# Kernel tuning notes

Measured on AMD Instinct MI355X. Metric: run time of the kernel, lower is better.

Reference implementation:

```python
import jax, jax.numpy as jnp
import numpy as np
import math

EPS = 1e-06
C_CONST = 2.0 + EPS
CHUNK = 128


def _features(xc, omega, W_poly, quad_nodes):
    # xc: (B,H,t,D) -> poly:(B,H,t,P), prf:(R,B,H,t,M)
    xn = xc / jnp.clip(jnp.linalg.norm(xc, axis=-1, keepdims=True), 1e-12)  # F.normalize
    poly = jnp.einsum('bhtd,hdp->bhtp', xn, W_poly)
    proj = jnp.einsum('bhtd,rhdm->rbhtm', xn, omega)
    s = quad_nodes[:, None, None, None, None]
    sqrt2s = jnp.sqrt(2.0 * jnp.clip(s, 0.0))
    M = omega.shape[-1]
    prf = jnp.exp(jnp.clip(proj * sqrt2s - s, -20.0, 20.0)) / math.sqrt(M)
    return poly, prf


def setup_inputs() -> dict:
    key = jax.random.key(0)
    ks = jax.random.split(key, 6)
    B, T, E, H, D, M, R, P = 1, 1024, 512, 8, 64, 8, 1, 32
    x = jax.random.normal(ks[0], (B, T, E), jnp.float32)
    W_qkv = jax.random.normal(ks[1], (3 * E, E), jnp.float32) / math.sqrt(E)
    b_qkv = jnp.zeros((3 * E,), jnp.float32)
    W_out = jax.random.normal(ks[2], (E, E), jnp.float32) / math.sqrt(E)
    b_out = jnp.zeros((E,), jnp.float32)
    omega = jax.random.normal(ks[3], (R, H, D, M), jnp.float32)
    W_poly = jax.random.normal(ks[4], (H, D, P), jnp.float32) / math.sqrt(D)
    nodes, weights = np.polynomial.laguerre.laggauss(R)
    quad_nodes = jnp.asarray(nodes, jnp.float32) / C_CONST
    quad_weights = jnp.asarray(weights, jnp.float32) / C_CONST
    return {"x": x, "W_qkv": W_qkv, "b_qkv": b_qkv, "W_out": W_out, "b_out": b_out,
            "omega": omega, "W_poly": W_poly, "quad_nodes": quad_nodes, "quad_weights": quad_weights}


def reference(x, W_qkv, b_qkv, W_out, b_out, omega, W_poly, quad_nodes, quad_weights):
    B, T, E = x.shape
    R, H, D, M = omega.shape
    P = W_poly.shape[-1]
    qkv = x @ W_qkv.T + b_qkv
    q, k, v = jnp.split(qkv, 3, axis=-1)

    def to_chunks(a):
        # (B,T,E) -> (Nc,B,H,chunk,D)
        return a.reshape(B, T, H, D).transpose(0, 2, 1, 3).reshape(B, H, T // CHUNK, CHUNK, D).transpose(2, 0, 1, 3, 4)

    qc, kc, vc = map(to_chunks, (q, k, v))
    sqw = jnp.sqrt(jnp.clip(quad_weights, 0.0))[:, None, None, None, None]
    kv0 = jnp.zeros((R, B, H, P, M, D), jnp.float32)
    k0 = jnp.zeros((R, B, H, P, M), jnp.float32)

    def step(carry, inp):
        kv_state, k_state = carry
        qch, kch, vch = inp
        q_poly, q_prf = _features(qch, omega, W_poly, quad_nodes)
        k_poly, k_prf = _features(kch, omega, W_poly, quad_nodes)
        q_prf = q_prf * sqw
        k_prf = k_prf * sqw
        q_outer = jnp.einsum('bhtp,rbhtm->rbhtpm', q_poly, q_prf)
        k_outer = jnp.einsum('bhtp,rbhtm->rbhtpm', k_poly, k_prf)
        kv_prod = jnp.einsum('rbhtpm,bhtd->rbhtpmd', k_outer, vch)
        kv_cur = jnp.cumsum(kv_prod, axis=3) + kv_state[:, :, :, None]
        k_cur = jnp.cumsum(k_outer, axis=3) + k_state[:, :, :, None]
        ctx = jnp.einsum('rbhtpm,rbhtpmd->bhtd', q_outer, kv_cur)  # sums over r too
        den = jnp.einsum('rbhtpm,rbhtpm->bht', q_outer, k_cur)
        out = ctx / jnp.clip(den, 1e-06)[..., None]
        return (kv_cur[:, :, :, -1], k_cur[:, :, :, -1]), out

    _, outs = jax.lax.scan(step, (kv0, k0), (qc, kc, vc))  # (Nc,B,H,chunk,D)
    out = outs.transpose(1, 2, 0, 3, 4).reshape(B, H, T, D).transpose(0, 2, 1, 3).reshape(B, T, E)
    return out @ W_out.T + b_out
```

## Files before the change

kernel.cpp:

```cpp
#include <hip/hip_runtime.h>
#include <math.h>


__global__ __launch_bounds__(256) void gemm_part_kernel(
    const float* __restrict__ A, const float* __restrict__ W,
    float* __restrict__ part, int M, int N, int K, int Kc)
{
    __shared__ float a_t[2][16][68];
    __shared__ float w_t[2][16][68];
    const int tid = threadIdx.x;
    const int n0 = blockIdx.x * 64;
    const int m0 = blockIdx.y * 64;
    const int sk = blockIdx.z;
    const int kb = sk * Kc;
    const int tx = tid & 15, ty = tid >> 4;
    const int lrow = tid >> 2;
    const int lk4  = (tid & 3) * 4;
    float acc[4][4];
#pragma unroll
    for (int i = 0; i < 4; ++i)
#pragma unroll
        for (int j = 0; j < 4; ++j) acc[i][j] = 0.f;

    const float* Ap = &A[(m0 + lrow) * K + kb + lk4];
    const float* Wp = &W[(n0 + lrow) * K + kb + lk4];
    float4 ra = *(const float4*)Ap;
    float4 rw = *(const float4*)Wp;
    a_t[0][lk4 + 0][lrow] = ra.x; a_t[0][lk4 + 1][lrow] = ra.y;
    a_t[0][lk4 + 2][lrow] = ra.z; a_t[0][lk4 + 3][lrow] = ra.w;
    w_t[0][lk4 + 0][lrow] = rw.x; w_t[0][lk4 + 1][lrow] = rw.y;
    w_t[0][lk4 + 2][lrow] = rw.z; w_t[0][lk4 + 3][lrow] = rw.w;
    __syncthreads();

    int cur = 0;
    for (int k0 = 16; k0 <= Kc; k0 += 16) {
        const bool more = (k0 < Kc);
        if (more) {
            ra = *(const float4*)(Ap + k0);
            rw = *(const float4*)(Wp + k0);
        }
#pragma unroll
        for (int k = 0; k < 16; ++k) {
            float4 af = *(const float4*)&a_t[cur][k][ty * 4];
            float4 wf = *(const float4*)&w_t[cur][k][tx * 4];
            acc[0][0] += af.x * wf.x; acc[0][1] += af.x * wf.y;
            acc[0][2] += af.x * wf.z; acc[0][3] += af.x * wf.w;
            acc[1][0] += af.y * wf.x; acc[1][1] += af.y * wf.y;
            acc[1][2] += af.y * wf.z; acc[1][3] += af.y * wf.w;
            acc[2][0] += af.z * wf.x; acc[2][1] += af.z * wf.y;
            acc[2][2] += af.z * wf.z; acc[2][3] += af.z * wf.w;
            acc[3][0] += af.w * wf.x; acc[3][1] += af.w * wf.y;
            acc[3][2] += af.w * wf.z; acc[3][3] += af.w * wf.w;
        }
        if (more) {
            const int nxt = cur ^ 1;
            a_t[nxt][lk4 + 0][lrow] = ra.x; a_t[nxt][lk4 + 1][lrow] = ra.y;
            a_t[nxt][lk4 + 2][lrow] = ra.z; a_t[nxt][lk4 + 3][lrow] = ra.w;
            w_t[nxt][lk4 + 0][lrow] = rw.x; w_t[nxt][lk4 + 1][lrow] = rw.y;
            w_t[nxt][lk4 + 2][lrow] = rw.z; w_t[nxt][lk4 + 3][lrow] = rw.w;
            __syncthreads();
            cur = nxt;
        }
    }
#pragma unroll
    for (int i = 0; i < 4; ++i) {
        float4 o = make_float4(acc[i][0], acc[i][1], acc[i][2], acc[i][3]);
        *(float4*)&part[((size_t)sk * M + m0 + ty * 4 + i) * N + n0 + tx * 4] = o;
    }
}

__global__ __launch_bounds__(256) void reduce_bias_kernel(
    const float* __restrict__ part, const float* __restrict__ bias,
    float* __restrict__ C, int MN, int N, int S)
{
    const int i4 = (blockIdx.x * 256 + threadIdx.x) * 4;
    if (i4 >= MN) return;
    float4 acc = *(const float4*)&part[i4];
    for (int s = 1; s < S; ++s) {
        float4 p = *(const float4*)&part[(size_t)s * MN + i4];
        acc.x += p.x; acc.y += p.y; acc.z += p.z; acc.w += p.w;
    }
    float4 b = *(const float4*)&bias[i4 % N];
    acc.x += b.x; acc.y += b.y; acc.z += b.z; acc.w += b.w;
    *(float4*)&C[i4] = acc;
}

__global__ __launch_bounds__(256) void features_kernel(
    const float* __restrict__ qkv, const float* __restrict__ omega,
    const float* __restrict__ W_poly, const float* __restrict__ qn,
    const float* __restrict__ qw, float* __restrict__ phi_q,
    float* __restrict__ phi_k)
{
    __shared__ float xn[4][2][64];
    __shared__ float poly[4][2][32];
    __shared__ float prf[4][2][8];
    const int tid = threadIdx.x;
    const int w = tid >> 6;
    const int lane = tid & 63;
    const int item = blockIdx.x * 4 + w;
    const int h = item >> 10;
    const int t = item & 1023;

    float xq = qkv[t * 1536 + h * 64 + lane];
    float xk = qkv[t * 1536 + 512 + h * 64 + lane];
    float sq = xq * xq, sk = xk * xk;
#pragma unroll
    for (int o = 32; o; o >>= 1) { sq += __shfl_xor(sq, o); sk += __shfl_xor(sk, o); }
    float xnq = xq / fmaxf(sqrtf(sq), 1e-12f);
    float xnk = xk / fmaxf(sqrtf(sk), 1e-12f);
    xn[w][0][lane] = xnq;
    xn[w][1][lane] = xnk;
    __syncthreads();

    {
        const int which = lane >> 5;
        const int p = lane & 31;
        float pacc = 0.f;
#pragma unroll 8
        for (int d = 0; d < 64; ++d)
            pacc += xn[w][which][d] * W_poly[(h * 64 + d) * 32 + p];
        poly[w][which][p] = pacc;
    }
    if (lane < 16) {
        const int wh2 = lane >> 3, m = lane & 7;
        float pr = 0.f;
#pragma unroll 8
        for (int d = 0; d < 64; ++d)
            pr += xn[w][wh2][d] * omega[(h * 64 + d) * 8 + m];
        float s0 = qn[0];
        float sqrt2s = sqrtf(2.f * fmaxf(s0, 0.f));
        float sqw = sqrtf(fmaxf(qw[0], 0.f));
        float z = fminf(fmaxf(pr * sqrt2s - s0, -20.f), 20.f);
        prf[w][wh2][m] = expf(z) * 0.3535533905932738f * sqw;
    }
    __syncthreads();

    const int pp = lane >> 1;
    const int mb = (lane & 1) * 4;
    float qp = poly[w][0][pp], kp = poly[w][1][pp];
    float4 oq, ok;
    oq.x = qp * prf[w][0][mb + 0]; oq.y = qp * prf[w][0][mb + 1];
    oq.z = qp * prf[w][0][mb + 2]; oq.w = qp * prf[w][0][mb + 3];
    ok.x = kp * prf[w][1][mb + 0]; ok.y = kp * prf[w][1][mb + 1];
    ok.z = kp * prf[w][1][mb + 2]; ok.w = kp * prf[w][1][mb + 3];
    *(float4*)&phi_q[((h << 10) + t) * 256 + lane * 4] = oq;
    *(float4*)&phi_k[((h << 10) + t) * 256 + lane * 4] = ok;
}

__global__ __launch_bounds__(256) void chunksum_kernel(
    const float* __restrict__ phi_k, const float* __restrict__ qkv,
    float* __restrict__ S_chunk, float* __restrict__ z_chunk)
{
    __shared__ float pk[128][64];
    __shared__ float vv[128][64];
    const int tid = threadIdx.x;
    const int h  = blockIdx.x >> 5;
    const int c  = (blockIdx.x >> 2) & 7;
    const int fg = blockIdx.x & 3;
    const int f0 = fg * 64;

#pragma unroll
    for (int i = 0; i < 8; ++i) {
        int e4 = i * 256 + tid;
        int s = e4 >> 4;
        int f4 = (e4 & 15) * 4;
        *(float4*)&pk[s][f4] =
            *(const float4*)&phi_k[((h << 10) + c * 128 + s) * 256 + f0 + f4];
    }
#pragma unroll
    for (int i = 0; i < 8; ++i) {
        int e4 = i * 256 + tid;
        int s = e4 >> 4;
        int d4 = (e4 & 15) * 4;
        *(float4*)&vv[s][d4] =
            *(const float4*)&qkv[(c * 128 + s) * 1536 + 1024 + h * 64 + d4];
    }
    __syncthreads();

    const int tx = tid & 15;
    const int ty = tid >> 4;
    float acc[4][4];
#pragma unroll
    for (int i = 0; i < 4; ++i)
#pragma unroll
        for (int j = 0; j < 4; ++j) acc[i][j] = 0.f;

    for (int s = 0; s < 128; ++s) {
        float4 pv = *(const float4*)&pk[s][ty * 4];
        float4 v4 = *(const float4*)&vv[s][tx * 4];
        acc[0][0] += pv.x * v4.x; acc[0][1] += pv.x * v4.y;
        acc[0][2] += pv.x * v4.z; acc[0][3] += pv.x * v4.w;
        acc[1][0] += pv.y * v4.x; acc[1][1] += pv.y * v4.y;
        acc[1][2] += pv.y * v4.z; acc[1][3] += pv.y * v4.w;
        acc[2][0] += pv.z * v4.x; acc[2][1] += pv.z * v4.y;
        acc[2][2] += pv.z * v4.z; acc[2][3] += pv.z * v4.w;
        acc[3][0] += pv.w * v4.x; acc[3][1] += pv.w * v4.y;
        acc[3][2] += pv.w * v4.z; acc[3][3] += pv.w * v4.w;
    }

    if (tid < 64) {
        float zacc = 0.f;
        for (int s = 0; s < 128; ++s) zacc += pk[s][tid];
        z_chunk[(h * 8 + c) * 256 + f0 + tid] = zacc;
    }

#pragma unroll
    for (int i = 0; i < 4; ++i) {
        float4 o = make_float4(acc[i][0], acc[i][1], acc[i][2], acc[i][3]);
        *(float4*)&S_chunk[((h * 8 + c) * 256 + f0 + ty * 4 + i) * 64 + tx * 4] = o;
    }
}

__global__ __launch_bounds__(256) void scan_kernel(
    const float* __restrict__ S_chunk, const float* __restrict__ z_chunk,
    float* __restrict__ S_prev, float* __restrict__ z_prev)
{
    int gid = blockIdx.x * 256 + threadIdx.x;
    if (gid < 8 * 256 * 64) {
        int h = gid >> 14;
        int r = gid & 16383;
        float acc = 0.f;
#pragma unroll
        for (int c = 0; c < 8; ++c) {
            int idx = ((h * 8 + c) << 14) + r;
            S_prev[idx] = acc;
            acc += S_chunk[idx];
        }
    }
    if (gid < 2048) {
        int h = gid >> 8, f = gid & 255;
        float acc = 0.f;
#pragma unroll
        for (int c = 0; c < 8; ++c) {
            int idx = (h * 8 + c) * 256 + f;
            z_prev[idx] = acc;
            acc += z_chunk[idx];
        }
    }
}

__global__ __launch_bounds__(512, 1) void attn_kernel(
    const float* __restrict__ phi_q, const float* __restrict__ phi_k,
    const float* __restrict__ qkv, const float* __restrict__ S_prev,
    const float* __restrict__ z_prev, float* __restrict__ attn)
{
    __shared__ float v_lds[128 * 64];
    __shared__ float A_lds[32 * 132];
    __shared__ float phq_t[32][36];
    __shared__ float phk_t[32][132];
    __shared__ float Sst[32][68];
    __shared__ float ctx_lds[32][64];
    __shared__ float z_lds[256];
    __shared__ float den_lds[32];
    const int tid = threadIdx.x;
    const int h = blockIdx.x >> 3, c = blockIdx.x & 7;
    const int tb = blockIdx.y * 32;
    const int SMAX = tb + 32;

    const int hc128 = (h << 10) + c * 128;
    const int hcS   = (h * 8 + c) * 256;

    for (int e4 = tid; e4 < SMAX * 16; e4 += 512) {
        int s = e4 >> 4;
        int d4 = (e4 & 15) * 4;
        *(float4*)&v_lds[s * 64 + d4] =
            *(const float4*)&qkv[(c * 128 + s) * 1536 + 1024 + h * 64 + d4];
    }
    if (tid < 256) z_lds[tid] = z_prev[hcS + tid];

    const int fidx = tid & 31;
    const int srow = tid >> 5;
    const int frow = tid >> 6;
    const int sdd  = tid & 63;

    const int tt = tid >> 5, ss = tid & 31;
    const bool ssActive = (ss * 4) < SMAX;
    const int u = tid & 255;
    const int d = u & 63, tg = u >> 6;

    float acc[4][4];
    float acc2[8];
    float den_acc = 0.f;
#pragma unroll
    for (int i = 0; i < 4; ++i)
#pragma unroll
        for (int j = 0; j < 4; ++j) acc[i][j] = 0.f;
#pragma unroll
    for (int i = 0; i < 8; ++i) acc2[i] = 0.f;

    float r_q0, r_q1, r_k[8], r_s[4];
#define LOAD_SLICE(F0)                                                        \
    do {                                                                      \
        r_q0 = phi_q[((hc128 + tb + srow) << 8) + (F0) + fidx];               \
        r_q1 = phi_q[((hc128 + tb + srow + 16) << 8) + (F0) + fidx];          \
        _Pragma("unroll")                                                     \
        for (int k = 0; k < 8; ++k) {                                         \
            int s_ = srow + 16 * k;                                           \
            r_k[k] = (s_ < SMAX) ? phi_k[((hc128 + s_) << 8) + (F0) + fidx]   \
                                 : 0.f;                                       \
        }                                                                     \
        _Pragma("unroll")                                                     \
        for (int k = 0; k < 4; ++k)                                           \
            r_s[k] = S_prev[((hcS + (F0) + frow + 8 * k) << 6) + sdd];        \
    } while (0)

    LOAD_SLICE(0);

    for (int ft = 0; ft < 8; ++ft) {
        const int f0 = ft * 32;
        __syncthreads();
        phq_t[fidx][srow]      = r_q0;
        phq_t[fidx][srow + 16] = r_q1;
#pragma unroll
        for (int k = 0; k < 8; ++k) phk_t[fidx][srow + 16 * k] = r_k[k];
#pragma unroll
        for (int k = 0; k < 4; ++k) Sst[frow + 8 * k][sdd] = r_s[k];
        __syncthreads();
        if (ft < 7) LOAD_SLICE(f0 + 32);

        if (tid < 256) {
            if (ssActive) {
#pragma unroll 4
                for (int f = 0; f < 32; ++f) {
                    float4 av = *(const float4*)&phq_t[f][tt * 4];
                    float4 bv = *(const float4*)&phk_t[f][ss * 4];
                    acc[0][0] += av.x * bv.x; acc[0][1] += av.x * bv.y;
                    acc[0][2] += av.x * bv.z; acc[0][3] += av.x * bv.w;
                    acc[1][0] += av.y * bv.x; acc[1][1] += av.y * bv.y;
                    acc[1][2] += av.y * bv.z; acc[1][3] += av.y * bv.w;
                    acc[2][0] += av.z * bv.x; acc[2][1] += av.z * bv.y;
                    acc[2][2] += av.z * bv.z; acc[2][3] += av.z * bv.w;
                    acc[3][0] += av.w * bv.x; acc[3][1] += av.w * bv.y;
                    acc[3][2] += av.w * bv.z; acc[3][3] += av.w * bv.w;
                }
            }
        } else {
#pragma unroll 4
            for (int f = 0; f < 32; ++f) {
                float sval = Sst[f][d];
                float4 a0 = *(const float4*)&phq_t[f][tg * 8];
                float4 a1 = *(const float4*)&phq_t[f][tg * 8 + 4];
                acc2[0] += a0.x * sval; acc2[1] += a0.y * sval;
                acc2[2] += a0.z * sval; acc2[3] += a0.w * sval;
                acc2[4] += a1.x * sval; acc2[5] += a1.y * sval;
                acc2[6] += a1.z * sval; acc2[7] += a1.w * sval;
            }
            if (u < 32) {
#pragma unroll
                for (int f = 0; f < 32; ++f)
                    den_acc += phq_t[f][u] * z_lds[f0 + f];
            }
        }
    }
#undef LOAD_SLICE

    if (tid < 256) {
        if (ssActive) {
#pragma unroll
            for (int i = 0; i < 4; ++i) {
                float4 o = make_float4(acc[i][0], acc[i][1], acc[i][2], acc[i][3]);
                *(float4*)&A_lds[(tt * 4 + i) * 132 + ss * 4] = o;
            }
        }
    } else {
#pragma unroll
        for (int i = 0; i < 8; ++i)
            ctx_lds[tg * 8 + i][d] = acc2[i];
        if (u < 32) den_lds[u] = den_acc;
    }
    __syncthreads();

    const int dd = tid & 63;
    const int rg = tid >> 6;
#pragma unroll
    for (int i = 0; i < 4; ++i) {
        int tl = rg * 4 + i;
        int tcr = tb + tl;
        float ctx = ctx_lds[tl][dd];
        float den = den_lds[tl];
        for (int s = 0; s <= tcr; ++s) {
            float a = A_lds[tl * 132 + s];
            ctx += a * v_lds[s * 64 + dd];
            den += a;
        }
        attn[(c * 128 + tcr) * 512 + h * 64 + dd] = ctx / fmaxf(den, 1e-6f);
    }
}

extern "C" void kernel_launch(void* const* d_in, const int* in_sizes, int n_in,
                              void* d_out, int out_size, void* d_ws, size_t ws_size,
                              hipStream_t stream)
{
    const float* x      = (const float*)d_in[0];
    const float* W_qkv  = (const float*)d_in[1];
    const float* b_qkv  = (const float*)d_in[2];
    const float* W_out  = (const float*)d_in[3];
    const float* b_out  = (const float*)d_in[4];
    const float* omega  = (const float*)d_in[5];
    const float* W_poly = (const float*)d_in[6];
    const float* qn     = (const float*)d_in[7];
    const float* qw     = (const float*)d_in[8];
    float* out = (float*)d_out;

    float* ws     = (float*)d_ws;
    float* qkv    = ws;
    float* phi_q  = qkv + 1572864;
    float* phi_k  = phi_q + 2097152;
    float* S_c    = phi_k + 2097152;
    float* z_c    = S_c + 1048576;
    float* S_p    = z_c + 16384;
    float* z_p    = S_p + 1048576;
    float* attn   = z_p + 16384;
    float* p_qkv  = attn + 524288;
    float* p_out  = p_qkv + 3145728;

    gemm_part_kernel<<<dim3(24, 16, 2), 256, 0, stream>>>(x, W_qkv, p_qkv, 1024, 1536, 512, 256);
    reduce_bias_kernel<<<1536, 256, 0, stream>>>(p_qkv, b_qkv, qkv, 1572864, 1536, 2);
    features_kernel<<<2048, 256, 0, stream>>>(qkv, omega, W_poly, qn, qw, phi_q, phi_k);
    chunksum_kernel<<<256, 256, 0, stream>>>(phi_k, qkv, S_c, z_c);
    scan_kernel<<<512, 256, 0, stream>>>(S_c, z_c, S_p, z_p);
    attn_kernel<<<dim3(64, 4), 512, 0, stream>>>(phi_q, phi_k, qkv, S_p, z_p, attn);
    gemm_part_kernel<<<dim3(8, 16, 4), 256, 0, stream>>>(attn, W_out, p_out, 1024, 512, 512, 128);
    reduce_bias_kernel<<<512, 256, 0, stream>>>(p_out, b_out, out, 524288, 512, 4);
}
```

Measured before the change: 168.9 us.

## Halve attention query tile, read V directly from global, deepen QKV split-K

The attention kernel now processes 16 query rows per block instead of 32, doubling the grid to 512 blocks. It drops the shared-memory V staging in favour of strided global reads, and it allows two blocks per CU. The QKV projection GEMM moves from split-K 2 to split-K 4 with a larger partial buffer. The goal is more parallelism and occupancy on a small problem, paid for with more redundant phi_k/S loads, uncoalesced V reads, and a heavier reduction pass.

```diff
diff --git a/kernel.cpp b/kernel.cpp
--- a/kernel.cpp
+++ b/kernel.cpp
@@ -239,33 +239,26 @@
     }
 }
 
-__global__ __launch_bounds__(512, 1) void attn_kernel(
+__global__ __launch_bounds__(512, 2) void attn_kernel(
     const float* __restrict__ phi_q, const float* __restrict__ phi_k,
     const float* __restrict__ qkv, const float* __restrict__ S_prev,
     const float* __restrict__ z_prev, float* __restrict__ attn)
 {
-    __shared__ float v_lds[128 * 64];
-    __shared__ float A_lds[32 * 132];
-    __shared__ float phq_t[32][36];
+    __shared__ float A_lds[16 * 132];
+    __shared__ float phq_t[32][20];
     __shared__ float phk_t[32][132];
     __shared__ float Sst[32][68];
-    __shared__ float ctx_lds[32][64];
+    __shared__ float ctx_lds[16][64];
     __shared__ float z_lds[256];
-    __shared__ float den_lds[32];
+    __shared__ float den_lds[16];
     const int tid = threadIdx.x;
     const int h = blockIdx.x >> 3, c = blockIdx.x & 7;
-    const int tb = blockIdx.y * 32;
-    const int SMAX = tb + 32;
+    const int tb = blockIdx.y * 16;
+    const int SMAX = tb + 16;
 
     const int hc128 = (h << 10) + c * 128;
     const int hcS   = (h * 8 + c) * 256;
 
-    for (int e4 = tid; e4 < SMAX * 16; e4 += 512) {
-        int s = e4 >> 4;
-        int d4 = (e4 & 15) * 4;
-        *(float4*)&v_lds[s * 64 + d4] =
-            *(const float4*)&qkv[(c * 128 + s) * 1536 + 1024 + h * 64 + d4];
-    }
     if (tid < 256) z_lds[tid] = z_prev[hcS + tid];
 
     const int fidx = tid & 31;
@@ -273,26 +266,26 @@
     const int frow = tid >> 6;
     const int sdd  = tid & 63;
 
-    const int tt = tid >> 5, ss = tid & 31;
+    const int tt = tid >> 5;
+    const int ss = tid & 31;
     const bool ssActive = (ss * 4) < SMAX;
     const int u = tid & 255;
     const int d = u & 63, tg = u >> 6;
 
-    float acc[4][4];
-    float acc2[8];
+    float acc[2][4];
+    float acc2[4];
     float den_acc = 0.f;
 #pragma unroll
-    for (int i = 0; i < 4; ++i)
+    for (int i = 0; i < 2; ++i)
 #pragma unroll
         for (int j = 0; j < 4; ++j) acc[i][j] = 0.f;
 #pragma unroll
-    for (int i = 0; i < 8; ++i) acc2[i] = 0.f;
-
-    float r_q0, r_q1, r_k[8], r_s[4];
+    for (int i = 0; i < 4; ++i) acc2[i] = 0.f;
+
+    float r_q0, r_k[8], r_s[4];
 #define LOAD_SLICE(F0)                                                        \
     do {                                                                      \
         r_q0 = phi_q[((hc128 + tb + srow) << 8) + (F0) + fidx];               \
-        r_q1 = phi_q[((hc128 + tb + srow + 16) << 8) + (F0) + fidx];          \
         _Pragma("unroll")                                                     \
         for (int k = 0; k < 8; ++k) {                                         \
             int s_ = srow + 16 * k;                                           \
@@ -309,8 +302,7 @@
     for (int ft = 0; ft < 8; ++ft) {
         const int f0 = ft * 32;
         __syncthreads();
-        phq_t[fidx][srow]      = r_q0;
-        phq_t[fidx][srow + 16] = r_q1;
+        phq_t[fidx][srow] = r_q0;
 #pragma unroll
         for (int k = 0; k < 8; ++k) phk_t[fidx][srow + 16 * k] = r_k[k];
 #pragma unroll
@@ -322,30 +314,24 @@
             if (ssActive) {
 #pragma unroll 4
                 for (int f = 0; f < 32; ++f) {
-                    float4 av = *(const float4*)&phq_t[f][tt * 4];
+                    float a0 = phq_t[f][tt * 2];
+                    float a1 = phq_t[f][tt * 2 + 1];
                     float4 bv = *(const float4*)&phk_t[f][ss * 4];
-                    acc[0][0] += av.x * bv.x; acc[0][1] += av.x * bv.y;
-                    acc[0][2] += av.x * bv.z; acc[0][3] += av.x * bv.w;
-                    acc[1][0] += av.y * bv.x; acc[1][1] += av.y * bv.y;
-                    acc[1][2] += av.y * bv.z; acc[1][3] += av.y * bv.w;
-                    acc[2][0] += av.z * bv.x; acc[2][1] += av.z * bv.y;
-                    acc[2][2] += av.z * bv.z; acc[2][3] += av.z * bv.w;
-                    acc[3][0] += av.w * bv.x; acc[3][1] += av.w * bv.y;
-                    acc[3][2] += av.w * bv.z; acc[3][3] += av.w * bv.w;
+                    acc[0][0] += a0 * bv.x; acc[0][1] += a0 * bv.y;
+                    acc[0][2] += a0 * bv.z; acc[0][3] += a0 * bv.w;
+                    acc[1][0] += a1 * bv.x; acc[1][1] += a1 * bv.y;
+                    acc[1][2] += a1 * bv.z; acc[1][3] += a1 * bv.w;
                 }
             }
         } else {
 #pragma unroll 4
             for (int f = 0; f < 32; ++f) {
                 float sval = Sst[f][d];
-                float4 a0 = *(const float4*)&phq_t[f][tg * 8];
-                float4 a1 = *(const float4*)&phq_t[f][tg * 8 + 4];
-                acc2[0] += a0.x * sval; acc2[1] += a0.y * sval;
-                acc2[2] += a0.z * sval; acc2[3] += a0.w * sval;
-                acc2[4] += a1.x * sval; acc2[5] += a1.y * sval;
-                acc2[6] += a1.z * sval; acc2[7] += a1.w * sval;
+                float4 a = *(const float4*)&phq_t[f][tg * 4];
+                acc2[0] += a.x * sval; acc2[1] += a.y * sval;
+                acc2[2] += a.z * sval; acc2[3] += a.w * sval;
             }
-            if (u < 32) {
+            if (u < 16) {
 #pragma unroll
                 for (int f = 0; f < 32; ++f)
                     den_acc += phq_t[f][u] * z_lds[f0 + f];
@@ -357,30 +343,31 @@
     if (tid < 256) {
         if (ssActive) {
 #pragma unroll
-            for (int i = 0; i < 4; ++i) {
+            for (int i = 0; i < 2; ++i) {
                 float4 o = make_float4(acc[i][0], acc[i][1], acc[i][2], acc[i][3]);
-                *(float4*)&A_lds[(tt * 4 + i) * 132 + ss * 4] = o;
+                *(float4*)&A_lds[(tt * 2 + i) * 132 + ss * 4] = o;
             }
         }
     } else {
 #pragma unroll
-        for (int i = 0; i < 8; ++i)
-            ctx_lds[tg * 8 + i][d] = acc2[i];
-        if (u < 32) den_lds[u] = den_acc;
+        for (int i = 0; i < 4; ++i)
+            ctx_lds[tg * 4 + i][d] = acc2[i];
+        if (u < 16) den_lds[u] = den_acc;
     }
     __syncthreads();
 
     const int dd = tid & 63;
     const int rg = tid >> 6;
-#pragma unroll
-    for (int i = 0; i < 4; ++i) {
-        int tl = rg * 4 + i;
+    const float* vp = qkv + (size_t)(c * 128) * 1536 + 1024 + h * 64 + dd;
+#pragma unroll
+    for (int i = 0; i < 2; ++i) {
+        int tl = rg * 2 + i;
         int tcr = tb + tl;
         float ctx = ctx_lds[tl][dd];
         float den = den_lds[tl];
         for (int s = 0; s <= tcr; ++s) {
             float a = A_lds[tl * 132 + s];
-            ctx += a * v_lds[s * 64 + dd];
+            ctx += a * vp[(size_t)s * 1536];
             den += a;
         }
         attn[(c * 128 + tcr) * 512 + h * 64 + dd] = ctx / fmaxf(den, 1e-6f);
@@ -412,14 +399,14 @@
     float* z_p    = S_p + 1048576;
     float* attn   = z_p + 16384;
     float* p_qkv  = attn + 524288;
-    float* p_out  = p_qkv + 3145728;
-
-    gemm_part_kernel<<<dim3(24, 16, 2), 256, 0, stream>>>(x, W_qkv, p_qkv, 1024, 1536, 512, 256);
-    reduce_bias_kernel<<<1536, 256, 0, stream>>>(p_qkv, b_qkv, qkv, 1572864, 1536, 2);
+    float* p_out  = p_qkv + 6291456;
+
+    gemm_part_kernel<<<dim3(24, 16, 4), 256, 0, stream>>>(x, W_qkv, p_qkv, 1024, 1536, 512, 128);
+    reduce_bias_kernel<<<1536, 256, 0, stream>>>(p_qkv, b_qkv, qkv, 1572864, 1536, 4);
     features_kernel<<<2048, 256, 0, stream>>>(qkv, omega, W_poly, qn, qw, phi_q, phi_k);
     chunksum_kernel<<<256, 256, 0, stream>>>(phi_k, qkv, S_c, z_c);
     scan_kernel<<<512, 256, 0, stream>>>(S_c, z_c, S_p, z_p);
-    attn_kernel<<<dim3(64, 4), 512, 0, stream>>>(phi_q, phi_k, qkv, S_p, z_p, attn);
+    attn_kernel<<<dim3(64, 8), 512, 0, stream>>>(phi_q, phi_k, qkv, S_p, z_p, attn);
     gemm_part_kernel<<<dim3(8, 16, 4), 256, 0, stream>>>(attn, W_out, p_out, 1024, 512, 512, 128);
     reduce_bias_kernel<<<512, 256, 0, stream>>>(p_out, b_out, out, 524288, 512, 4);
 }
```

After: 178.3 us. 1.06x slower.
